# Kernel optimization log

Measured on AMD Instinct MI355X. Metric: run time of the kernel, lower is better.

Reference implementation:

```python
import jax, jax.numpy as jnp
import numpy as np

H, W, N, B = 64, 64, 512, 32


def setup_inputs() -> dict:
    key = jax.random.key(0)
    k1, _ = jax.random.split(key)
    data = jax.random.normal(k1, (B, N, 8), dtype=jnp.float32)
    opacity = jnp.ones((N, 1), dtype=jnp.float32)
    return {"data": data, "opacity": opacity}


def reference(data, opacity):
    # data: (B, N, 8) -> image (B, 3, H, W)
    xy = jnp.tanh(data[..., :2])                       # (B,N,2) in [-1,1]
    scale = jnp.abs(data[..., 2:4]) + 0.3              # (B,N,2)
    theta = jax.nn.sigmoid(data[..., 4]) * (2.0 * np.pi)  # (B,N)
    color = data[..., 5:8]                             # (B,N,3)

    # NDC -> pixel coords (GaussianImage convention)
    px = 0.5 * ((xy[..., 0] + 1.0) * W - 1.0)          # (B,N)
    py = 0.5 * ((xy[..., 1] + 1.0) * H - 1.0)

    # 2D covariance: R diag(s^2) R^T
    c, s = jnp.cos(theta), jnp.sin(theta)
    s0sq, s1sq = scale[..., 0] ** 2, scale[..., 1] ** 2
    cov_a = c * c * s0sq + s * s * s1sq                # (B,N)
    cov_b = c * s * (s0sq - s1sq)
    cov_c = s * s * s0sq + c * c * s1sq
    det = cov_a * cov_c - cov_b * cov_b
    # conic = inverse covariance
    con_a = cov_c / det
    con_b = -cov_b / det
    con_c = cov_a / det

    xs = jnp.arange(W, dtype=jnp.float32)              # pixel x coords
    ys = jnp.arange(H, dtype=jnp.float32)
    dx = xs[None, None, :] - px[..., None]             # (B,N,W)
    dy = ys[None, None, :] - py[..., None]             # (B,N,H)

    # sigma = 0.5*(A dx^2 + C dy^2) + B dx dy  -> (B,N,H,W)
    sigma = (0.5 * con_a[..., None, None] * (dx[:, :, None, :] ** 2)
             + 0.5 * con_c[..., None, None] * (dy[:, :, :, None] ** 2)
             + con_b[..., None, None] * dy[:, :, :, None] * dx[:, :, None, :])
    alpha = opacity[None, :, 0, None, None] * jnp.exp(-sigma)  # (B,N,H,W)

    # sum blending: out[b,c,h,w] = sum_n alpha[b,n,h,w] * color[b,n,c]
    img = jnp.einsum('bnhw,bnc->bchw', alpha, color)
    return img
```

## Files before the change

### kernel.cpp

```cpp
#include <hip/hip_runtime.h>
#include <math.h>

#define Hh 64
#define Ww 64
#define Nn 512
#define Bb 32
#define NPIX (Hh * Ww)
#define TCUT 16.0f

__global__ __launch_bounds__(256) void gs_fused(const float* __restrict__ data,
                                                const float* __restrict__ opacity,
                                                float* __restrict__ out) {
    __shared__ float4 sA[Nn];
    __shared__ float4 sB[Nn];
    __shared__ float  sC[Nn];
    __shared__ float4 sD[Nn];
    __shared__ short  slist[4][Nn / 2];
    __shared__ float  comb[2][3][64];

    int bid    = blockIdx.x;
    int region = bid & 31;
    int b      = bid >> 5;
    int t      = threadIdx.x;
    int base   = b * Nn;

#pragma unroll
    for (int j = 0; j < Nn / 256; ++j) {
        int n = j * 256 + t;
        const float4* dp = (const float4*)(data) + (size_t)(base + n) * 2;
        float4 d0 = dp[0];
        float4 d1 = dp[1];

        float xy0 = tanhf(d0.x);
        float xy1 = tanhf(d0.y);
        float s0 = fabsf(d0.z) + 0.3f;
        float s1 = fabsf(d0.w) + 0.3f;
        float theta = (1.0f / (1.0f + expf(-d1.x))) * (2.0f * (float)M_PI);
        float c = cosf(theta);
        float s = sinf(theta);

        float px = 0.5f * ((xy0 + 1.0f) * (float)Ww - 1.0f);
        float py = 0.5f * ((xy1 + 1.0f) * (float)Hh - 1.0f);

        float s0sq = s0 * s0, s1sq = s1 * s1;
        float cov_a = c * c * s0sq + s * s * s1sq;
        float cov_b = c * s * (s0sq - s1sq);
        float cov_c = s * s * s0sq + c * c * s1sq;
        float det = cov_a * cov_c - cov_b * cov_b;
        float inv = 1.0f / det;
        float con_a = cov_c * inv;
        float con_b = -cov_b * inv;
        float con_c = cov_a * inv;

        const float L2E = 1.4426950408889634f;
        float a2 = -0.5f * con_a * L2E;
        float b2 = -con_b * L2E;
        float c2 = -0.5f * con_c * L2E;

        float q1 = -(2.0f * a2 * px + b2 * py);
        float q2 = -(2.0f * c2 * py + b2 * px);
        float q0 = a2 * px * px + b2 * px * py + c2 * py * py;

        float det2 = 4.0f * a2 * c2 - b2 * b2;
        float rinv = 1.0f / det2;
        float xext = sqrtf(fmaxf(4.0f * TCUT * (-c2) * rinv, 0.0f));
        float yext = sqrtf(fmaxf(4.0f * TCUT * (-a2) * rinv, 0.0f));

        float op = opacity[n];

        sA[n] = make_float4(q0, q1, q2, a2);
        sB[n] = make_float4(b2, c2, op * d1.y, op * d1.z);
        sC[n] = op * d1.w;
        sD[n] = make_float4(px, py, xext, yext);
    }
    __syncthreads();

    int w    = t >> 6;
    int lane = t & 63;
    int qx0  = (region & 3) * 16 + (w & 1) * 8;
    int qy0  = (region >> 2) * 8;
    int nh   = w >> 1;
    float fxq0 = (float)qx0, fxq1 = (float)(qx0 + 7);
    float fyq0 = (float)qy0, fyq1 = (float)(qy0 + 7);

    short* wl = slist[w];
    int cnt = 0;
#pragma unroll
    for (int r = 0; r < 4; ++r) {
        int ln = nh * 256 + r * 64 + lane;
        float4 D = sD[ln];
        bool keep = (D.x + D.z >= fxq0) && (D.x - D.z <= fxq1) &&
                    (D.y + D.w >= fyq0) && (D.y - D.w <= fyq1);
        unsigned long long m = __ballot(keep);
        int pos = (int)__popcll(m & ((1ull << lane) - 1ull));
        if (keep) wl[cnt + pos] = (short)ln;
        cnt += (int)__popcll(m);
    }

    float fx = (float)(qx0 + (lane & 7));
    float fy = (float)(qy0 + (lane >> 3));
    float fx2 = fx * fx;
    float fxy = fx * fy;
    float fy2 = fy * fy;

    float accr = 0.0f, accg = 0.0f, accb = 0.0f;
#pragma unroll 4
    for (int i = 0; i < cnt; ++i) {
        int ln = wl[i];
        float4 A  = sA[ln];
        float4 Bv = sB[ln];
        float  ob = sC[ln];
        float sgm = fmaf(A.y, fx, A.x);
        sgm = fmaf(A.z, fy, sgm);
        sgm = fmaf(A.w, fx2, sgm);
        sgm = fmaf(Bv.x, fxy, sgm);
        sgm = fmaf(Bv.y, fy2, sgm);
        float e = __builtin_amdgcn_exp2f(sgm);
        accr = fmaf(e, Bv.z, accr);
        accg = fmaf(e, Bv.w, accg);
        accb = fmaf(e, ob, accb);
    }

    if (w >= 2) {
        comb[w - 2][0][lane] = accr;
        comb[w - 2][1][lane] = accg;
        comb[w - 2][2][lane] = accb;
    }
    __syncthreads();
    if (w < 2) {
        accr += comb[w][0][lane];
        accg += comb[w][1][lane];
        accb += comb[w][2][lane];
        int pix = (qy0 + (lane >> 3)) * Ww + qx0 + (lane & 7);
        size_t obase = (size_t)b * 3 * NPIX + (size_t)pix;
        out[obase]            = accr;
        out[obase + NPIX]     = accg;
        out[obase + 2 * NPIX] = accb;
    }
}

extern "C" void kernel_launch(void* const* d_in, const int* in_sizes, int n_in,
                              void* d_out, int out_size, void* d_ws, size_t ws_size,
                              hipStream_t stream) {
    const float* data    = (const float*)d_in[0];
    const float* opacity = (const float*)d_in[1];
    float* out = (float*)d_out;

    gs_fused<<<Bb * 32, 256, 0, stream>>>(data, opacity, out);
}
```

Before: 12.71 us.

## Use one 8x8 tile per block with Gaussian split across waves, plus fast-math intrinsics

The grid doubles to 64 blocks per batch image, each covering one 8x8 pixel tile. Each of the four waves culls and accumulates a quarter of the Gaussians, and wave 0 sums the partial colours. The per-Gaussian setup replaces tanhf, expf, sinf/cosf, division and sqrt with AMDGCN hardware intrinsics (exp2, rcp, sin/cos in revolutions, sqrt) to make the preamble cheaper. The setup is still recomputed per block, so it now runs twice as often in total, and the approximate intrinsics lose a little precision.

```diff
diff --git a/kernel.cpp b/kernel.cpp
--- a/kernel.cpp
+++ b/kernel.cpp
@@ -8,6 +8,17 @@
 #define NPIX (Hh * Ww)
 #define TCUT 16.0f
 
+#define L2E 1.4426950408889634f
+
+__device__ __forceinline__ float fast_sigmoid(float x) {
+    float e = __builtin_amdgcn_exp2f(-x * L2E);
+    return __builtin_amdgcn_rcpf(1.0f + e);
+}
+__device__ __forceinline__ float fast_tanh(float x) {
+    float e = __builtin_amdgcn_exp2f(x * (-2.0f * L2E));
+    return fmaf(2.0f, __builtin_amdgcn_rcpf(1.0f + e), -1.0f);
+}
+
 __global__ __launch_bounds__(256) void gs_fused(const float* __restrict__ data,
                                                 const float* __restrict__ opacity,
                                                 float* __restrict__ out) {
@@ -15,14 +26,14 @@
     __shared__ float4 sB[Nn];
     __shared__ float  sC[Nn];
     __shared__ float4 sD[Nn];
-    __shared__ short  slist[4][Nn / 2];
-    __shared__ float  comb[2][3][64];
+    __shared__ short  slist[4][Nn / 4];
+    __shared__ float  comb[3][3][64];
 
-    int bid    = blockIdx.x;
-    int region = bid & 31;
-    int b      = bid >> 5;
-    int t      = threadIdx.x;
-    int base   = b * Nn;
+    int bid  = blockIdx.x;
+    int tile = bid & 63;
+    int b    = bid >> 6;
+    int t    = threadIdx.x;
+    int base = b * Nn;
 
 #pragma unroll
     for (int j = 0; j < Nn / 256; ++j) {
@@ -31,13 +42,13 @@
         float4 d0 = dp[0];
         float4 d1 = dp[1];
 
-        float xy0 = tanhf(d0.x);
-        float xy1 = tanhf(d0.y);
+        float xy0 = fast_tanh(d0.x);
+        float xy1 = fast_tanh(d0.y);
         float s0 = fabsf(d0.z) + 0.3f;
         float s1 = fabsf(d0.w) + 0.3f;
-        float theta = (1.0f / (1.0f + expf(-d1.x))) * (2.0f * (float)M_PI);
-        float c = cosf(theta);
-        float s = sinf(theta);
+        float u  = fast_sigmoid(d1.x);
+        float c  = __builtin_amdgcn_cosf(u);
+        float s  = __builtin_amdgcn_sinf(u);
 
         float px = 0.5f * ((xy0 + 1.0f) * (float)Ww - 1.0f);
         float py = 0.5f * ((xy1 + 1.0f) * (float)Hh - 1.0f);
@@ -47,12 +58,11 @@
         float cov_b = c * s * (s0sq - s1sq);
         float cov_c = s * s * s0sq + c * c * s1sq;
         float det = cov_a * cov_c - cov_b * cov_b;
-        float inv = 1.0f / det;
+        float inv = __builtin_amdgcn_rcpf(det);
         float con_a = cov_c * inv;
         float con_b = -cov_b * inv;
         float con_c = cov_a * inv;
 
-        const float L2E = 1.4426950408889634f;
         float a2 = -0.5f * con_a * L2E;
         float b2 = -con_b * L2E;
         float c2 = -0.5f * con_c * L2E;
@@ -62,9 +72,9 @@
         float q0 = a2 * px * px + b2 * px * py + c2 * py * py;
 
         float det2 = 4.0f * a2 * c2 - b2 * b2;
-        float rinv = 1.0f / det2;
-        float xext = sqrtf(fmaxf(4.0f * TCUT * (-c2) * rinv, 0.0f));
-        float yext = sqrtf(fmaxf(4.0f * TCUT * (-a2) * rinv, 0.0f));
+        float rinv = __builtin_amdgcn_rcpf(det2);
+        float xext = __builtin_amdgcn_sqrtf(fmaxf(4.0f * TCUT * (-c2) * rinv, 0.0f));
+        float yext = __builtin_amdgcn_sqrtf(fmaxf(4.0f * TCUT * (-a2) * rinv, 0.0f));
 
         float op = opacity[n];
 
@@ -77,17 +87,16 @@
 
     int w    = t >> 6;
     int lane = t & 63;
-    int qx0  = (region & 3) * 16 + (w & 1) * 8;
-    int qy0  = (region >> 2) * 8;
-    int nh   = w >> 1;
-    float fxq0 = (float)qx0, fxq1 = (float)(qx0 + 7);
-    float fyq0 = (float)qy0, fyq1 = (float)(qy0 + 7);
+    int tx0  = (tile & 7) * 8;
+    int ty0  = (tile >> 3) * 8;
+    float fxq0 = (float)tx0, fxq1 = (float)(tx0 + 7);
+    float fyq0 = (float)ty0, fyq1 = (float)(ty0 + 7);
 
     short* wl = slist[w];
     int cnt = 0;
 #pragma unroll
-    for (int r = 0; r < 4; ++r) {
-        int ln = nh * 256 + r * 64 + lane;
+    for (int r = 0; r < 2; ++r) {
+        int ln = w * 128 + r * 64 + lane;
         float4 D = sD[ln];
         bool keep = (D.x + D.z >= fxq0) && (D.x - D.z <= fxq1) &&
                     (D.y + D.w >= fyq0) && (D.y - D.w <= fyq1);
@@ -97,8 +106,8 @@
         cnt += (int)__popcll(m);
     }
 
-    float fx = (float)(qx0 + (lane & 7));
-    float fy = (float)(qy0 + (lane >> 3));
+    float fx = (float)(tx0 + (lane & 7));
+    float fy = (float)(ty0 + (lane >> 3));
     float fx2 = fx * fx;
     float fxy = fx * fy;
     float fy2 = fy * fy;
@@ -121,17 +130,17 @@
         accb = fmaf(e, ob, accb);
     }
 
-    if (w >= 2) {
-        comb[w - 2][0][lane] = accr;
-        comb[w - 2][1][lane] = accg;
-        comb[w - 2][2][lane] = accb;
+    if (w > 0) {
+        comb[w - 1][0][lane] = accr;
+        comb[w - 1][1][lane] = accg;
+        comb[w - 1][2][lane] = accb;
     }
     __syncthreads();
-    if (w < 2) {
-        accr += comb[w][0][lane];
-        accg += comb[w][1][lane];
-        accb += comb[w][2][lane];
-        int pix = (qy0 + (lane >> 3)) * Ww + qx0 + (lane & 7);
+    if (w == 0) {
+        accr += comb[0][0][lane] + comb[1][0][lane] + comb[2][0][lane];
+        accg += comb[0][1][lane] + comb[1][1][lane] + comb[2][1][lane];
+        accb += comb[0][2][lane] + comb[1][2][lane] + comb[2][2][lane];
+        int pix = (ty0 + (lane >> 3)) * Ww + tx0 + (lane & 7);
         size_t obase = (size_t)b * 3 * NPIX + (size_t)pix;
         out[obase]            = accr;
         out[obase + NPIX]     = accg;
@@ -146,5 +155,5 @@
     const float* opacity = (const float*)d_in[1];
     float* out = (float*)d_out;
 
-    gs_fused<<<Bb * 32, 256, 0, stream>>>(data, opacity, out);
+    gs_fused<<<Bb * 64, 256, 0, stream>>>(data, opacity, out);
 }
```

New measurement: 12.29 us. 3.3% less time.
